# Performance work log

Measured on AMD Instinct MI355X. Metric: run time of the kernel, lower is better.

The kernel has to match this reference:

```python
import jax, jax.numpy as jnp
import numpy as np

B, T, H = 4, 2048, 1024
BUD = 512
S = max(8, BUD)
S += S % 2
HALF = S // 2
LOC = max(H, 2 * BUD)


def setup_inputs() -> dict:
    key = jax.random.key(0)
    ks = jax.random.split(key, 16)
    def w(k, i, o):
        return jax.random.normal(k, (i, o), jnp.float32) / np.sqrt(i).astype(np.float32)
    return {
        "x": jax.random.normal(ks[0], (B, T, H), jnp.float32),
        "W_rf": w(ks[1], H, S), "W_ri": w(ks[2], H, S), "W_rv": w(ks[3], H, S),
        "W_rq": w(ks[4], H, S), "W_ro": w(ks[5], S, H),
        "W_sw": w(ks[6], H, S), "W_sg": w(ks[7], H, S), "W_som": w(ks[8], H, HALF),
        "W_sd": w(ks[9], H, S), "W_sq": w(ks[10], H, S), "W_so": w(ks[11], S, H),
        "W_up": w(ks[12], H, LOC), "W_gate": w(ks[13], H, LOC), "W_down": w(ks[14], LOC, H),
        "W_mix": w(ks[15], H, 3),
        "read_init": jnp.zeros((S,), jnp.float32),
        "stable_init": jnp.zeros((S,), jnp.float32),
    }


def reference(x, W_rf, W_ri, W_rv, W_rq, W_ro, W_sw, W_sg, W_som, W_sd, W_sq, W_so,
              W_up, W_gate, W_down, W_mix, read_init, stable_init):
    silu = jax.nn.silu
    # Precompute all per-token projections as batched GEMMs: [B,T,*]
    rf = jnp.tanh(x @ W_rf)                      # read forget
    rg = jax.nn.sigmoid(x @ W_ri)                # read input gate
    rc = silu(x @ W_rv)                          # read candidate
    omega = jnp.pi * jnp.tanh(x @ W_som)         # [B,T,HALF]
    cosw, sinw = jnp.cos(omega), jnp.sin(omega)
    damp = jnp.exp(-jax.nn.softplus(x @ W_sd))
    sg = jax.nn.sigmoid(x @ W_sg)
    sc = silu(x @ W_sw)

    def step(carry, inputs):
        rs, ss = carry
        rf_t, rg_t, rc_t, cw, sw_, dp, sg_t, sc_t = inputs
        rs = rf_t * rs + rg_t * rc_t
        even, odd = ss[:, :HALF], ss[:, HALF:]
        rot = jnp.concatenate([cw * even - sw_ * odd, sw_ * even + cw * odd], axis=-1)
        ss = dp * rot + sg_t * sc_t
        return (rs, ss), (rs, ss)

    init = (jnp.broadcast_to(read_init, (B, S)), jnp.broadcast_to(stable_init, (B, S)))
    seq = tuple(jnp.swapaxes(a, 0, 1) for a in (rf, rg, rc, cosw, sinw, damp, sg, sc))
    _, (rs_seq, ss_seq) = jax.lax.scan(step, init, seq)
    rs_seq = jnp.swapaxes(rs_seq, 0, 1)  # [B,T,S]
    ss_seq = jnp.swapaxes(ss_seq, 0, 1)

    read_f = silu((x @ W_rq) * rs_seq) @ W_ro
    stable_f = silu((x @ W_sq) * ss_seq) @ W_so
    local_f = ((x @ W_up) * silu(x @ W_gate)) @ W_down
    mw = jax.nn.softmax(x @ W_mix, axis=-1)  # [B,T,3]
    out = mw[..., 0:1] * read_f + mw[..., 1:2] * stable_f + mw[..., 2:3] * local_f
    return out
```

## Files before the change

### kernel.cpp

```cpp
#include <hip/hip_runtime.h>

#define B_    4
#define T_    2048
#define H_    1024
#define S_    512
#define HALF_ 256
#define LOC_  1024
#define BT_   8192
#define N1_   6400
#define K1_   1024
#define N2_   1024
#define K2_   2048
#define NCH_  32
#define LC_   64

typedef __attribute__((ext_vector_type(8))) short  bf16x8;
typedef __attribute__((ext_vector_type(4))) float  f32x4;
typedef __attribute__((ext_vector_type(4))) unsigned short u16x4;

__device__ __forceinline__ float b2f(unsigned short u) {
    union { unsigned i; float f; } v; v.i = ((unsigned)u) << 16; return v.f;
}
__device__ __forceinline__ unsigned short f2b(float f) {
    union { float f; unsigned i; } v; v.f = f;
    unsigned r = v.i + 0x7fffu + ((v.i >> 16) & 1u);
    return (unsigned short)(r >> 16);
}
__device__ __forceinline__ float rcp_(float x) { return __builtin_amdgcn_rcpf(x); }
__device__ __forceinline__ float sigm_(float v) { return rcp_(1.f + __expf(-v)); }
__device__ __forceinline__ float silu_(float v) { return v * rcp_(1.f + __expf(-v)); }
__device__ __forceinline__ float tanh_(float v) { return 1.f - 2.f * rcp_(1.f + __expf(2.f * v)); }

__device__ __forceinline__ void gload16(const void* g, void* l) {
    __builtin_amdgcn_global_load_lds(
        (const __attribute__((address_space(1))) void*)g,
        (__attribute__((address_space(3))) void*)l,
        16, 0, 0);
}

__global__ void pack_x_kernel(const float* __restrict__ x, unsigned short* __restrict__ xb) {
    int i = blockIdx.x * 256 + threadIdx.x;
    float4 a = ((const float4*)x)[i];
    u16x4 u;
    u.x = f2b(a.x); u.y = f2b(a.y); u.z = f2b(a.z); u.w = f2b(a.w);
    ((u16x4*)xb)[i] = u;
}

struct TOp { const float* src; int Kw; int Nw; int n_ofs; int k_ofs; int which; };
struct TOps { TOp v[14]; };

__global__ void pack_w_kernel(TOps ops, unsigned short* __restrict__ w1, unsigned short* __restrict__ w2) {
    TOp op = ops.v[blockIdx.z];
    int kt = blockIdx.x * 32, nt = blockIdx.y * 32;
    if (kt >= op.Kw || nt >= op.Nw) return;
    __shared__ float tile[32][33];
    int tx = threadIdx.x & 31, ty = threadIdx.x >> 5;
#pragma unroll
    for (int r = 0; r < 4; r++) {
        int k = kt + ty + r * 8;
        tile[ty + r * 8][tx] = op.src[(size_t)k * op.Nw + nt + tx];
    }
    __syncthreads();
    unsigned short* dst = op.which ? w2 : w1;
    int stride = op.which ? K2_ : K1_;
#pragma unroll
    for (int r = 0; r < 4; r++) {
        int n = nt + ty + r * 8;
        dst[(size_t)(op.n_ofs + n) * stride + op.k_ofs + kt + tx] = f2b(tile[tx][ty + r * 8]);
    }
}

__global__ void mix_kernel(const float* __restrict__ x, const float* __restrict__ Wm,
                           float4* __restrict__ mw) {
    int row  = blockIdx.x * 4 + (threadIdx.x >> 6);
    int lane = threadIdx.x & 63;
    const float* xr = x + (size_t)row * H_;
    float s0 = 0.f, s1 = 0.f, s2 = 0.f;
    for (int k = lane; k < H_; k += 64) {
        float xv = xr[k];
        s0 += xv * Wm[k * 3 + 0];
        s1 += xv * Wm[k * 3 + 1];
        s2 += xv * Wm[k * 3 + 2];
    }
#pragma unroll
    for (int off = 32; off; off >>= 1) {
        s0 += __shfl_down(s0, off);
        s1 += __shfl_down(s1, off);
        s2 += __shfl_down(s2, off);
    }
    if (lane == 0) {
        float m = fmaxf(s0, fmaxf(s1, s2));
        float e0 = __expf(s0 - m), e1 = __expf(s1 - m), e2 = __expf(s2 - m);
        float inv = 1.f / (e0 + e1 + e2);
        mw[row] = (float4){ e0 * inv, e1 * inv, e2 * inv, 0.f };
    }
}

#define STAGE(kt_, dA, dB) {          \
    gload16(aP0 + (kt_), (dA));       \
    gload16(aP1 + (kt_), (dA) + 512); \
    gload16(bP0 + (kt_), (dB));       \
    gload16(bP1 + (kt_), (dB) + 512); }

#define COMPUTE(sAr, sBr) {                                                            \
    bf16x8 af[4], bfv[4];                                                              \
    _Pragma("unroll")                                                                  \
    for (int m_ = 0; m_ < 4; m_++)                                                     \
        af[m_] = *(const bf16x8*)((sAr) + (wm + m_ * 16 + fr) * 32 + rsl);             \
    _Pragma("unroll")                                                                  \
    for (int n_ = 0; n_ < 4; n_++)                                                     \
        bfv[n_] = *(const bf16x8*)((sBr) + (wn + n_ * 16 + fr) * 32 + rsl);            \
    _Pragma("unroll")                                                                  \
    for (int m_ = 0; m_ < 4; m_++)                                                     \
        _Pragma("unroll")                                                              \
        for (int n_ = 0; n_ < 4; n_++)                                                 \
            acc[m_][n_] = __builtin_amdgcn_mfma_f32_16x16x32_bf16(af[m_], bfv[n_], acc[m_][n_], 0, 0, 0); }

template<int MODE>
__global__ __launch_bounds__(256, 3) void gemm_bf16(
    const unsigned short* __restrict__ A,
    const unsigned short* __restrict__ Bt,
    void* __restrict__ Cout,
    unsigned short* __restrict__ swb,
    const int M, const int N, const int K)
{
    __shared__ __align__(16) char smem[32768];
    unsigned short* sA0 = (unsigned short*)smem;
    unsigned short* sB0 = (unsigned short*)(smem + 8192);
    unsigned short* sA1 = (unsigned short*)(smem + 16384);
    unsigned short* sB1 = (unsigned short*)(smem + 24576);
    const int tid  = threadIdx.x;
    const int wid  = tid >> 6;
    const int lane = tid & 63;

    const int flat = blockIdx.y * gridDim.x + blockIdx.x;
    const int xcd  = flat & 7;
    const int ii   = flat >> 3;
    const int bm   = ((xcd << 3) + (ii & 7)) * 128;
    const int bn   = (ii >> 3) * 128;

    const int wm = (wid >> 1) * 64;
    const int wn = (wid & 1) * 64;

    f32x4 acc[4][4];
#pragma unroll
    for (int m = 0; m < 4; m++)
#pragma unroll
        for (int n = 0; n < 4; n++) acc[m][n] = (f32x4){0.f, 0.f, 0.f, 0.f};

    const int r0 = wid * 32 + (lane >> 2);
    const int sl = ((lane & 3) ^ ((r0 >> 1) & 3)) * 8;
    const unsigned short* aP0 = A  + (size_t)(bm + r0)      * K + sl;
    const unsigned short* aP1 = A  + (size_t)(bm + r0 + 16) * K + sl;
    const unsigned short* bP0 = Bt + (size_t)(bn + r0)      * K + sl;
    const unsigned short* bP1 = Bt + (size_t)(bn + r0 + 16) * K + sl;
    unsigned short* wA0 = sA0 + wid * 1024;
    unsigned short* wB0 = sB0 + wid * 1024;
    unsigned short* wA1 = sA1 + wid * 1024;
    unsigned short* wB1 = sB1 + wid * 1024;

    const int fr  = lane & 15;
    const int h   = lane >> 4;
    const int rsl = (h ^ ((fr >> 1) & 3)) * 8;
    const int nt  = K >> 5;

    STAGE(0, wA0, wB0);
    __syncthreads();
    for (int t = 0; t < nt; t += 2) {
        STAGE((t + 1) * 32, wA1, wB1);
        COMPUTE(sA0, sB0);
        __syncthreads();
        if (t + 2 < nt) STAGE((t + 2) * 32, wA0, wB0);
        COMPUTE(sA1, sB1);
        __syncthreads();
    }

    if (MODE == 0) {
        float* outp = (float*)Cout;
        float* wp = (float*)(smem + wid * 4608);
#pragma unroll
        for (int m = 0; m < 4; m++) {
#pragma unroll
            for (int n = 0; n < 4; n++)
#pragma unroll
                for (int r = 0; r < 4; r++)
                    wp[(h * 4 + r) * 68 + n * 16 + fr] = acc[m][n][r];
#pragma unroll
            for (int rnd = 0; rnd < 4; rnd++) {
                int lr = rnd * 4 + (lane >> 4);
                int lc = (lane & 15) * 4;
                float4 v = *(float4*)&wp[lr * 68 + lc];
                int grow = bm + wm + m * 16 + lr;
                int gcol = bn + wn + lc;
                *(float4*)&outp[(size_t)grow * N + gcol] = v;
            }
        }
    } else {
        int reg;
        if      (bn < 512)  reg = 0;
        else if (bn < 1024) reg = 1;
        else if (bn < 1536) reg = 2;
        else if (bn < 2048) reg = 3;
        else if (bn < 2560) reg = 2;
        else if (bn < 3072) reg = 1;
        else if (bn < 3584) reg = 4;
        else if (bn < 4096) reg = 3;
        else if (bn < 4352) reg = 5;
        else if (bn < 5376) reg = 3;
        else                reg = 2;

        unsigned short* proj = (unsigned short*)Cout;
        unsigned short* wp = (unsigned short*)(smem + wid * 2304);
        const int nsub = (reg == 5) ? 2 : 1;
#pragma unroll
        for (int m = 0; m < 4; m++) {
            for (int sub = 0; sub < nsub; sub++) {
#pragma unroll
                for (int n = 0; n < 4; n++)
#pragma unroll
                    for (int r = 0; r < 4; r++) {
                        float v = acc[m][n][r];
                        float o;
                        if      (reg == 0) o = tanh_(v);
                        else if (reg == 1) o = sigm_(v);
                        else if (reg == 2) o = silu_(v);
                        else if (reg == 3) o = v;
                        else if (reg == 4) o = sigm_(-v);
                        else {
                            float om = 3.14159265358979f * tanh_(v);
                            o = sub ? __sinf(om) : __cosf(om);
                        }
                        wp[(h * 4 + r) * 72 + n * 16 + fr] = f2b(o);
                    }
#pragma unroll
                for (int p = 0; p < 2; p++) {
                    int lr = p * 8 + (lane >> 3);
                    int lc = (lane & 7) * 8;
                    bf16x8 v = *(bf16x8*)(wp + lr * 72 + lc);
                    int grow = bm + wm + m * 16 + lr;
                    int gcol = bn + wn + lc;
                    if (sub == 0)
                        *(bf16x8*)(proj + (size_t)grow * N + gcol) = v;
                    else
                        *(bf16x8*)(swb + (size_t)grow * HALF_ + (gcol - 4096)) = v;
                }
            }
        }
    }
}

__global__ void scan_pass1(const unsigned short* __restrict__ proj, const unsigned short* __restrict__ swb,
                           float* __restrict__ rsP, float* __restrict__ rsY,
                           float4* __restrict__ ssM, float2* __restrict__ ssY) {
    const int c = blockIdx.x, b = blockIdx.y, z = blockIdx.z, tid = threadIdx.x;
    const int row0 = b * T_ + c * LC_;
    const unsigned short* base = proj + (size_t)row0 * N1_;
    if (z < 2) {
        const int s = z * 256 + tid;
        float P = 1.f, y = 0.f;
#pragma unroll 4
        for (int t = 0; t < LC_; t++) {
            const unsigned short* r = base + (size_t)t * N1_;
            float rf = b2f(r[s]);
            float rg = b2f(r[512 + s]);
            float rc = b2f(r[1024 + s]);
            y = rf * y + rg * rc;
            P *= rf;
        }
        int idx = (b * NCH_ + c) * S_ + s;
        rsP[idx] = P; rsY[idx] = y;
    } else {
        const int p = tid;
        const unsigned short* swr = swb + (size_t)row0 * HALF_;
        float m00 = 1.f, m01 = 0.f, m10 = 0.f, m11 = 1.f, y0 = 0.f, y1 = 0.f;
#pragma unroll 2
        for (int t = 0; t < LC_; t++) {
            const unsigned short* r = base + (size_t)t * N1_;
            float cw  = b2f(r[4096 + p]);
            float sw  = b2f(swr[(size_t)t * HALF_ + p]);
            float de  = b2f(r[3072 + p]);
            float dob = b2f(r[3328 + p]);
            float ge  = b2f(r[2560 + p]);
            float go  = b2f(r[2816 + p]);
            float ce  = b2f(r[2048 + p]);
            float co  = b2f(r[2304 + p]);
            float a = de * cw, bb = -de * sw, cc = dob * sw, dd = dob * cw;
            float ny0 = a * y0 + bb * y1 + ge * ce;
            float ny1 = cc * y0 + dd * y1 + go * co;
            y0 = ny0; y1 = ny1;
            float n00 = a * m00 + bb * m10, n01 = a * m01 + bb * m11;
            float n10 = cc * m00 + dd * m10, n11 = cc * m01 + dd * m11;
            m00 = n00; m01 = n01; m10 = n10; m11 = n11;
        }
        int idx = (b * NCH_ + c) * HALF_ + p;
        ssM[idx] = (float4){m00, m01, m10, m11};
        ssY[idx] = (float2){y0, y1};
    }
}

__global__ void scan_pass2(const float* __restrict__ rsP, const float* __restrict__ rsY,
                           const float4* __restrict__ ssM, const float2* __restrict__ ssY,
                           const float* __restrict__ read_init, const float* __restrict__ stable_init,
                           float* __restrict__ rsStart, float2* __restrict__ ssStart) {
    int id = blockIdx.x * 256 + threadIdx.x;
    if (id < B_ * S_) {
        int b = id / S_, s = id % S_;
        float st = read_init[s];
        for (int c = 0; c < NCH_; c++) {
            int idx = (b * NCH_ + c) * S_ + s;
            rsStart[idx] = st;
            st = rsP[idx] * st + rsY[idx];
        }
    } else {
        id -= B_ * S_;
        int b = id / HALF_, p = id % HALF_;
        float y0 = stable_init[p], y1 = stable_init[p + HALF_];
        for (int c = 0; c < NCH_; c++) {
            int idx = (b * NCH_ + c) * HALF_ + p;
            ssStart[idx] = (float2){y0, y1};
            float4 m = ssM[idx]; float2 u = ssY[idx];
            float ny0 = m.x * y0 + m.y * y1 + u.x;
            float ny1 = m.z * y0 + m.w * y1 + u.y;
            y0 = ny0; y1 = ny1;
        }
    }
}

__global__ void scan_pass3(const unsigned short* __restrict__ proj, const unsigned short* __restrict__ swb,
                           const float* __restrict__ rsStart, const float2* __restrict__ ssStart,
                           const float4* __restrict__ mw, unsigned short* __restrict__ G) {
    const int c = blockIdx.x, b = blockIdx.y, z = blockIdx.z, tid = threadIdx.x;
    const int row0 = b * T_ + c * LC_;
    const unsigned short* base = proj + (size_t)row0 * N1_;
    if (z < 2) {
        const int s = z * 256 + tid;
        float rs = rsStart[(b * NCH_ + c) * S_ + s];
#pragma unroll 4
        for (int t = 0; t < LC_; t++) {
            const size_t row = row0 + t;
            const unsigned short* r = base + (size_t)t * N1_;
            float rf = b2f(r[s]);
            float rg = b2f(r[512 + s]);
            float rc = b2f(r[1024 + s]);
            rs = rf * rs + rg * rc;
            float q  = b2f(r[1536 + s]);
            float zz = q * rs;
            G[row * 2048 + s] = f2b(mw[row].x * silu_(zz));
        }
    } else {
        const int p = tid;
        const unsigned short* swr = swb + (size_t)row0 * HALF_;
        float2 st = ssStart[(b * NCH_ + c) * HALF_ + p];
        float y0 = st.x, y1 = st.y;
#pragma unroll 2
        for (int t = 0; t < LC_; t++) {
            const size_t row = row0 + t;
            const unsigned short* r = base + (size_t)t * N1_;
            float cw  = b2f(r[4096 + p]);
            float sw  = b2f(swr[(size_t)t * HALF_ + p]);
            float de  = b2f(r[3072 + p]);
            float dob = b2f(r[3328 + p]);
            float ge  = b2f(r[2560 + p]);
            float go  = b2f(r[2816 + p]);
            float ce  = b2f(r[2048 + p]);
            float co  = b2f(r[2304 + p]);
            float a = de * cw, bb = -de * sw, cc = dob * sw, dd = dob * cw;
            float ny0 = a * y0 + bb * y1 + ge * ce;
            float ny1 = cc * y0 + dd * y1 + go * co;
            y0 = ny0; y1 = ny1;
            float qe = b2f(r[3584 + p]);
            float qo = b2f(r[3840 + p]);
            float w1v = mw[row].y;
            G[row * 2048 + 512 + p] = f2b(w1v * silu_(qe * y0));
            G[row * 2048 + 768 + p] = f2b(w1v * silu_(qo * y1));
        }
    }
}

__global__ void local_ew(const unsigned short* __restrict__ proj, const float4* __restrict__ mw,
                         unsigned short* __restrict__ G) {
    int i   = blockIdx.x * 256 + threadIdx.x;
    int row = i >> 7;
    int j   = (i & 127) * 8;
    bf16x8 up = *(const bf16x8*)(proj + (size_t)row * N1_ + 4352 + j);
    bf16x8 gs = *(const bf16x8*)(proj + (size_t)row * N1_ + 5376 + j);
    float m2 = mw[row].z;
    bf16x8 o;
#pragma unroll
    for (int e = 0; e < 8; e++)
        o[e] = (short)f2b(m2 * b2f((unsigned short)up[e]) * b2f((unsigned short)gs[e]));
    *(bf16x8*)(G + (size_t)row * 2048 + 1024 + j) = o;
}

extern "C" void kernel_launch(void* const* d_in, const int* in_sizes, int n_in,
                              void* d_out, int out_size, void* d_ws, size_t ws_size,
                              hipStream_t stream) {
    const float* x       = (const float*)d_in[0];
    const float* W_rf    = (const float*)d_in[1];
    const float* W_ri    = (const float*)d_in[2];
    const float* W_rv    = (const float*)d_in[3];
    const float* W_rq    = (const float*)d_in[4];
    const float* W_ro    = (const float*)d_in[5];
    const float* W_sw    = (const float*)d_in[6];
    const float* W_sg    = (const float*)d_in[7];
    const float* W_som   = (const float*)d_in[8];
    const float* W_sd    = (const float*)d_in[9];
    const float* W_sq    = (const float*)d_in[10];
    const float* W_so    = (const float*)d_in[11];
    const float* W_up    = (const float*)d_in[12];
    const float* W_gate  = (const float*)d_in[13];
    const float* W_down  = (const float*)d_in[14];
    const float* W_mix   = (const float*)d_in[15];
    const float* read_init   = (const float*)d_in[16];
    const float* stable_init = (const float*)d_in[17];

    char* ws = (char*)d_ws;
    size_t off = 0;
    auto alloc = [&](size_t bytes) -> void* {
        void* p = ws + off;
        off = (off + bytes + 255) & ~(size_t)255;
        return p;
    };
    unsigned short* xb   = (unsigned short*)alloc((size_t)BT_ * H_ * 2);
    unsigned short* w1   = (unsigned short*)alloc((size_t)N1_ * K1_ * 2);
    unsigned short* w2   = (unsigned short*)alloc((size_t)N2_ * K2_ * 2);
    unsigned short* proj = (unsigned short*)alloc((size_t)BT_ * N1_ * 2);
    unsigned short* swb  = (unsigned short*)alloc((size_t)BT_ * HALF_ * 2);
    float4*         mw   = (float4*)alloc((size_t)BT_ * 16);
    unsigned short* G    = (unsigned short*)alloc((size_t)BT_ * 2048 * 2);
    float*  rsP     = (float*) alloc((size_t)B_ * NCH_ * S_ * 4);
    float*  rsY     = (float*) alloc((size_t)B_ * NCH_ * S_ * 4);
    float4* ssM     = (float4*)alloc((size_t)B_ * NCH_ * HALF_ * 16);
    float2* ssY     = (float2*)alloc((size_t)B_ * NCH_ * HALF_ * 8);
    float*  rsStart = (float*) alloc((size_t)B_ * NCH_ * S_ * 4);
    float2* ssStart = (float2*)alloc((size_t)B_ * NCH_ * HALF_ * 8);
    if (off > ws_size) return;

    pack_x_kernel<<<(BT_ * H_ / 4) / 256, 256, 0, stream>>>(x, xb);

    TOps ops;
    int i = 0;
    auto add = [&](const float* s, int Kw, int Nw, int n_ofs, int k_ofs, int which) {
        ops.v[i].src = s; ops.v[i].Kw = Kw; ops.v[i].Nw = Nw;
        ops.v[i].n_ofs = n_ofs; ops.v[i].k_ofs = k_ofs; ops.v[i].which = which; i++;
    };
    add(W_rf,  1024,  512,    0,    0, 0);
    add(W_ri,  1024,  512,  512,    0, 0);
    add(W_rv,  1024,  512, 1024,    0, 0);
    add(W_rq,  1024,  512, 1536,    0, 0);
    add(W_sw,  1024,  512, 2048,    0, 0);
    add(W_sg,  1024,  512, 2560,    0, 0);
    add(W_sd,  1024,  512, 3072,    0, 0);
    add(W_sq,  1024,  512, 3584,    0, 0);
    add(W_som, 1024,  256, 4096,    0, 0);
    add(W_up,  1024, 1024, 4352,    0, 0);
    add(W_gate,1024, 1024, 5376,    0, 0);
    add(W_ro,   512, 1024,    0,    0, 1);
    add(W_so,   512, 1024,    0,  512, 1);
    add(W_down,1024, 1024,    0, 1024, 1);
    pack_w_kernel<<<dim3(32, 32, 14), 256, 0, stream>>>(ops, w1, w2);

    mix_kernel<<<BT_ / 4, 256, 0, stream>>>(x, W_mix, mw);

    gemm_bf16<1><<<dim3(N1_ / 128, BT_ / 128), 256, 0, stream>>>(xb, w1, (void*)proj, swb, BT_, N1_, K1_);

    scan_pass1<<<dim3(NCH_, B_, 3), 256, 0, stream>>>(proj, swb, rsP, rsY, ssM, ssY);
    scan_pass2<<<12, 256, 0, stream>>>(rsP, rsY, ssM, ssY, read_init, stable_init, rsStart, ssStart);
    scan_pass3<<<dim3(NCH_, B_, 3), 256, 0, stream>>>(proj, swb, rsStart, ssStart, mw, G);

    local_ew<<<(BT_ * LOC_ / 8) / 256, 256, 0, stream>>>(proj, mw, G);

    gemm_bf16<0><<<dim3(N2_ / 128, BT_ / 128), 256, 0, stream>>>(G, w2, d_out, nullptr, BT_, N2_, K2_);
}
```

Baseline: 282.1 us.

## Use 256x256-tile, 4-stage pipelined GEMM for the fused projection

Replaces the 128x128 double-buffered projection GEMM with a 512-thread kernel using 256x256 tiles and a four-buffer LDS ring with explicit vmcnt waits and barriers. The larger tile raises arithmetic intensity per byte loaded, and the deeper prefetch hides global latency. The MFMA block is wrapped in raised wave priority. The output GEMM is split into its own non-templated kernel. The cost is a 128KB LDS footprint and more accumulator registers, which limit occupancy. N1=6400 gives 25 column tiles, so wave quantization shifts.

After: 324.5 us. +15.0%, slower.

```diff
diff --git a/kernel.cpp b/kernel.cpp
--- a/kernel.cpp
+++ b/kernel.cpp
@@ -38,6 +38,10 @@
         16, 0, 0);
 }
 
+#define SB0 __builtin_amdgcn_sched_barrier(0)
+#define BARR __builtin_amdgcn_s_barrier()
+#define WAITVN(n) asm volatile("s_waitcnt vmcnt(" #n ")" ::: "memory")
+
 __global__ void pack_x_kernel(const float* __restrict__ x, unsigned short* __restrict__ xb) {
     int i = blockIdx.x * 256 + threadIdx.x;
     float4 a = ((const float4*)x)[i];
@@ -93,6 +97,135 @@
         float e0 = __expf(s0 - m), e1 = __expf(s1 - m), e2 = __expf(s2 - m);
         float inv = 1.f / (e0 + e1 + e2);
         mw[row] = (float4){ e0 * inv, e1 * inv, e2 * inv, 0.f };
+    }
+}
+
+__global__ __launch_bounds__(512, 2) void gemm256_proj(
+    const unsigned short* __restrict__ A,
+    const unsigned short* __restrict__ Bt,
+    unsigned short* __restrict__ proj,
+    unsigned short* __restrict__ swb,
+    const int M, const int N, const int K)
+{
+    __shared__ __align__(16) unsigned short smem[65536];
+    const int tid  = threadIdx.x;
+    const int wid  = tid >> 6;
+    const int lane = tid & 63;
+    const int wr = wid >> 2;
+    const int wc = wid & 3;
+    const int fr = lane & 15;
+    const int h  = lane >> 4;
+
+    const int flat = blockIdx.y * gridDim.x + blockIdx.x;
+    const int xcd  = flat & 7;
+    const int ii   = flat >> 3;
+    const int mpx  = gridDim.y >> 3;
+    const int bm   = (xcd * mpx + (ii % mpx)) * 256;
+    const int bn   = (ii / mpx) * 256;
+
+    f32x4 acc[8][4];
+#pragma unroll
+    for (int m = 0; m < 8; m++)
+#pragma unroll
+        for (int n = 0; n < 4; n++) acc[m][n] = (f32x4){0.f, 0.f, 0.f, 0.f};
+
+    const int rl  = lane >> 2;
+    const int ssw = ((lane & 3) ^ (rl & 3)) * 8;
+    const unsigned short* aS0 = A  + (size_t)(bm + wid * 32 + rl) * K + ssw;
+    const unsigned short* aS1 = aS0 + (size_t)16 * K;
+    const unsigned short* bS0 = Bt + (size_t)(bn + wid * 32 + rl) * K + ssw;
+    const unsigned short* bS1 = bS0 + (size_t)16 * K;
+    const int stgO = wid * 1024;
+
+    const int rsw = (h ^ (fr & 3)) * 8;
+    const int NT  = K >> 5;
+
+#define ISSUE4(tt, cc) {                                        \
+        const size_t ko = (size_t)(tt) * 32;                    \
+        unsigned short* dA = smem + (cc) * 16384 + stgO;        \
+        unsigned short* dB = smem + (cc) * 16384 + 8192 + stgO; \
+        gload16(aS0 + ko, dA); gload16(aS1 + ko, dA + 512);     \
+        gload16(bS0 + ko, dB); gload16(bS1 + ko, dB + 512); }
+
+    ISSUE4(0, 0); ISSUE4(1, 1); ISSUE4(2, 2);
+    SB0; WAITVN(8); SB0; BARR; SB0;
+
+    for (int t = 0; t < NT; ++t) {
+        const int c = t & 3;
+        const unsigned short* bufA = smem + c * 16384;
+        const unsigned short* bufB = bufA + 8192;
+        bf16x8 af[8], bfv[4];
+#pragma unroll
+        for (int m = 0; m < 8; m++)
+            af[m] = *(const bf16x8*)(bufA + (wr * 128 + m * 16 + fr) * 32 + rsw);
+#pragma unroll
+        for (int n = 0; n < 4; n++)
+            bfv[n] = *(const bf16x8*)(bufB + (wc * 64 + n * 16 + fr) * 32 + rsw);
+        __builtin_amdgcn_s_setprio(1);
+#pragma unroll
+        for (int m = 0; m < 8; m++)
+#pragma unroll
+            for (int n = 0; n < 4; n++)
+                acc[m][n] = __builtin_amdgcn_mfma_f32_16x16x32_bf16(af[m], bfv[n], acc[m][n], 0, 0, 0);
+        __builtin_amdgcn_s_setprio(0);
+        SB0; BARR; SB0;
+        const int rem = NT - 1 - t;
+        if (rem >= 3)      { ISSUE4(t + 3, (t + 3) & 3); SB0; WAITVN(8); }
+        else if (rem == 2) { WAITVN(4); }
+        else if (rem == 1) { WAITVN(0); }
+        if (rem >= 1) { SB0; BARR; SB0; }
+    }
+#undef ISSUE4
+
+    const int col0w = bn + wc * 64;
+    int reg;
+    if      (col0w < 512)  reg = 0;
+    else if (col0w < 1024) reg = 1;
+    else if (col0w < 1536) reg = 2;
+    else if (col0w < 2048) reg = 3;
+    else if (col0w < 2560) reg = 2;
+    else if (col0w < 3072) reg = 1;
+    else if (col0w < 3584) reg = 4;
+    else if (col0w < 4096) reg = 3;
+    else if (col0w < 4352) reg = 5;
+    else if (col0w < 5376) reg = 3;
+    else                   reg = 2;
+
+    unsigned short* wls = smem + wid * 1152;
+    const int nsub = (reg == 5) ? 2 : 1;
+#pragma unroll
+    for (int m = 0; m < 8; m++) {
+        for (int sub = 0; sub < nsub; sub++) {
+#pragma unroll
+            for (int n = 0; n < 4; n++)
+#pragma unroll
+                for (int r = 0; r < 4; r++) {
+                    float v = acc[m][n][r];
+                    float o;
+                    if      (reg == 0) o = tanh_(v);
+                    else if (reg == 1) o = sigm_(v);
+                    else if (reg == 2) o = silu_(v);
+                    else if (reg == 3) o = v;
+                    else if (reg == 4) o = sigm_(-v);
+                    else {
+                        float om = 3.14159265358979f * tanh_(v);
+                        o = sub ? __sinf(om) : __cosf(om);
+                    }
+                    wls[(h * 4 + r) * 72 + n * 16 + fr] = f2b(o);
+                }
+#pragma unroll
+            for (int p = 0; p < 2; p++) {
+                int lr = p * 8 + (lane >> 3);
+                int lc = (lane & 7) * 8;
+                bf16x8 v8 = *(bf16x8*)(wls + lr * 72 + lc);
+                int grow = bm + wr * 128 + m * 16 + lr;
+                int gcol = bn + wc * 64 + lc;
+                if (sub == 0)
+                    *(bf16x8*)(proj + (size_t)grow * N + gcol) = v8;
+                else
+                    *(bf16x8*)(swb + (size_t)grow * HALF_ + (gcol - 4096)) = v8;
+            }
+        }
     }
 }
 
@@ -116,12 +249,10 @@
         for (int n_ = 0; n_ < 4; n_++)                                                 \
             acc[m_][n_] = __builtin_amdgcn_mfma_f32_16x16x32_bf16(af[m_], bfv[n_], acc[m_][n_], 0, 0, 0); }
 
-template<int MODE>
-__global__ __launch_bounds__(256, 3) void gemm_bf16(
+__global__ __launch_bounds__(256, 3) void gemm_f32out(
     const unsigned short* __restrict__ A,
     const unsigned short* __restrict__ Bt,
-    void* __restrict__ Cout,
-    unsigned short* __restrict__ swb,
+    float* __restrict__ outp,
     const int M, const int N, const int K)
 {
     __shared__ __align__(16) char smem[32768];
@@ -175,76 +306,22 @@
         __syncthreads();
     }
 
-    if (MODE == 0) {
-        float* outp = (float*)Cout;
-        float* wp = (float*)(smem + wid * 4608);
-#pragma unroll
-        for (int m = 0; m < 4; m++) {
-#pragma unroll
-            for (int n = 0; n < 4; n++)
-#pragma unroll
-                for (int r = 0; r < 4; r++)
-                    wp[(h * 4 + r) * 68 + n * 16 + fr] = acc[m][n][r];
-#pragma unroll
-            for (int rnd = 0; rnd < 4; rnd++) {
-                int lr = rnd * 4 + (lane >> 4);
-                int lc = (lane & 15) * 4;
-                float4 v = *(float4*)&wp[lr * 68 + lc];
-                int grow = bm + wm + m * 16 + lr;
-                int gcol = bn + wn + lc;
-                *(float4*)&outp[(size_t)grow * N + gcol] = v;
-            }
-        }
-    } else {
-        int reg;
-        if      (bn < 512)  reg = 0;
-        else if (bn < 1024) reg = 1;
-        else if (bn < 1536) reg = 2;
-        else if (bn < 2048) reg = 3;
-        else if (bn < 2560) reg = 2;
-        else if (bn < 3072) reg = 1;
-        else if (bn < 3584) reg = 4;
-        else if (bn < 4096) reg = 3;
-        else if (bn < 4352) reg = 5;
-        else if (bn < 5376) reg = 3;
-        else                reg = 2;
-
-        unsigned short* proj = (unsigned short*)Cout;
-        unsigned short* wp = (unsigned short*)(smem + wid * 2304);
-        const int nsub = (reg == 5) ? 2 : 1;
-#pragma unroll
-        for (int m = 0; m < 4; m++) {
-            for (int sub = 0; sub < nsub; sub++) {
-#pragma unroll
-                for (int n = 0; n < 4; n++)
-#pragma unroll
-                    for (int r = 0; r < 4; r++) {
-                        float v = acc[m][n][r];
-                        float o;
-                        if      (reg == 0) o = tanh_(v);
-                        else if (reg == 1) o = sigm_(v);
-                        else if (reg == 2) o = silu_(v);
-                        else if (reg == 3) o = v;
-                        else if (reg == 4) o = sigm_(-v);
-                        else {
-                            float om = 3.14159265358979f * tanh_(v);
-                            o = sub ? __sinf(om) : __cosf(om);
-                        }
-                        wp[(h * 4 + r) * 72 + n * 16 + fr] = f2b(o);
-                    }
-#pragma unroll
-                for (int p = 0; p < 2; p++) {
-                    int lr = p * 8 + (lane >> 3);
-                    int lc = (lane & 7) * 8;
-                    bf16x8 v = *(bf16x8*)(wp + lr * 72 + lc);
-                    int grow = bm + wm + m * 16 + lr;
-                    int gcol = bn + wn + lc;
-                    if (sub == 0)
-                        *(bf16x8*)(proj + (size_t)grow * N + gcol) = v;
-                    else
-                        *(bf16x8*)(swb + (size_t)grow * HALF_ + (gcol - 4096)) = v;
-                }
-            }
+    float* wp = (float*)(smem + wid * 4608);
+#pragma unroll
+    for (int m = 0; m < 4; m++) {
+#pragma unroll
+        for (int n = 0; n < 4; n++)
+#pragma unroll
+            for (int r = 0; r < 4; r++)
+                wp[(h * 4 + r) * 68 + n * 16 + fr] = acc[m][n][r];
+#pragma unroll
+        for (int rnd = 0; rnd < 4; rnd++) {
+            int lr = rnd * 4 + (lane >> 4);
+            int lc = (lane & 15) * 4;
+            float4 v = *(float4*)&wp[lr * 68 + lc];
+            int grow = bm + wm + m * 16 + lr;
+            int gcol = bn + wn + lc;
+            *(float4*)&outp[(size_t)grow * N + gcol] = v;
         }
     }
 }
@@ -462,7 +539,7 @@
 
     mix_kernel<<<BT_ / 4, 256, 0, stream>>>(x, W_mix, mw);
 
-    gemm_bf16<1><<<dim3(N1_ / 128, BT_ / 128), 256, 0, stream>>>(xb, w1, (void*)proj, swb, BT_, N1_, K1_);
+    gemm256_proj<<<dim3(N1_ / 256, BT_ / 256), 512, 0, stream>>>(xb, w1, proj, swb, BT_, N1_, K1_);
 
     scan_pass1<<<dim3(NCH_, B_, 3), 256, 0, stream>>>(proj, swb, rsP, rsY, ssM, ssY);
     scan_pass2<<<12, 256, 0, stream>>>(rsP, rsY, ssM, ssY, read_init, stable_init, rsStart, ssStart);
@@ -470,5 +547,5 @@
 
     local_ew<<<(BT_ * LOC_ / 8) / 256, 256, 0, stream>>>(proj, mw, G);
 
-    gemm_bf16<0><<<dim3(N2_ / 128, BT_ / 128), 256, 0, stream>>>(G, w2, d_out, nullptr, BT_, N2_, K2_);
-}
+    gemm_f32out<<<dim3(N2_ / 128, BT_ / 128), 256, 0, stream>>>(G, w2, (float*)d_out, BT_, N2_, K2_);
+}
```
